# Kernel optimization log

Hardware: AMD Instinct MI355X
Metric: run time of the kernel (lower is better)

## Reference

```python
import jax, jax.numpy as jnp
import numpy as np

NUM_CODES = 8192
EMBED_DIM = 256
N_TOKENS = 65536
COMMITMENT_COST = 0.25


def setup_inputs() -> dict:
    key = jax.random.key(0)
    k1, k2 = jax.random.split(key)
    inputs = jax.random.normal(k1, (N_TOKENS, EMBED_DIM), dtype=jnp.float32)
    # torch init: uniform(-1/num_codes, 1/num_codes); use normal-scale equivalent via uniform
    weight = jax.random.uniform(k2, (NUM_CODES, EMBED_DIM), dtype=jnp.float32,
                                minval=-1.0 / NUM_CODES, maxval=1.0 / NUM_CODES)
    return {"inputs": inputs, "weight": weight}


def reference(inputs, weight):
    inputs_sq = jnp.sum(inputs * inputs, axis=1, keepdims=True)      # (N, 1)
    embed_sq = jnp.sum(weight * weight, axis=1)                      # (K,)
    distances = inputs_sq + embed_sq - 2.0 * (inputs @ weight.T)     # (N, K)
    indices = jnp.argmin(distances, axis=1)                          # (N,)
    quantized = jnp.take(weight, indices, axis=0)                    # (N, D)

    codebook_loss = jnp.mean((quantized - jax.lax.stop_gradient(inputs)) ** 2)
    commit_loss = jnp.mean((inputs - jax.lax.stop_gradient(quantized)) ** 2)
    vq_loss = codebook_loss + COMMITMENT_COST * commit_loss

    # straight-through estimator
    quantized_st = inputs + jax.lax.stop_gradient(quantized - inputs)
    return quantized_st, indices, vq_loss, codebook_loss, commit_loss
```

## Files before the change

### kernel.cpp

```cpp
#include <hip/hip_runtime.h>

#define N_TOK  65536
#define N_CODE 8192
#define DIM    256

typedef _Float16 f16;
typedef _Float16 f16x8 __attribute__((ext_vector_type(8)));
typedef float    f32x4 __attribute__((ext_vector_type(4)));

__global__ __launch_bounds__(256) void rowsq2_kernel(const float* __restrict__ W,
                                                     const float* __restrict__ X,
                                                     float* __restrict__ esq,
                                                     float* __restrict__ sxq) {
    int row  = blockIdx.x * 4 + (threadIdx.x >> 6);
    int lane = threadIdx.x & 63;
    const float* src;
    float* dst;
    if (row < N_CODE) { src = W + (size_t)row * DIM;            dst = esq + row; }
    else              { src = X + (size_t)(row - N_CODE) * DIM; dst = sxq + (row - N_CODE); }
    float4 v = ((const float4*)src)[lane];
    float s = v.x * v.x + v.y * v.y + v.z * v.z + v.w * v.w;
#pragma unroll
    for (int off = 32; off; off >>= 1) s += __shfl_down(s, off, 64);
    if (lane == 0) *dst = s;
}

__global__ __launch_bounds__(256) void splitw_t_kernel(const float* __restrict__ W,
                                                       f16* __restrict__ W1t,
                                                       f16* __restrict__ W2t,
                                                       double* __restrict__ accum) {
    if (blockIdx.x == 0 && threadIdx.x < 128) accum[threadIdx.x] = 0.0;
    int g = blockIdx.x * 256 + threadIdx.x;
    int o = g >> 13;
    int c = g & 8191;
    const float* p = W + (size_t)c * DIM + o * 8;
    float4 v0 = ((const float4*)p)[0];
    float4 v1 = ((const float4*)p)[1];
    float e[8] = {v0.x, v0.y, v0.z, v0.w, v1.x, v1.y, v1.z, v1.w};
    union { f16 h[8]; uint4 u; } p1, p2;
#pragma unroll
    for (int i = 0; i < 8; ++i) {
        float ws = e[i] * 16384.0f;
        f16 w1 = (f16)ws;
        float r = (ws - (float)w1) * 2048.0f;
        p1.h[i] = w1; p2.h[i] = (f16)r;
    }
    size_t byteoff = (size_t)o * 131072 + (size_t)c * 16;
    *(uint4*)((char*)W1t + byteoff) = p1.u;
    *(uint4*)((char*)W2t + byteoff) = p2.u;
}

__global__ __launch_bounds__(256, 2) void argmin_mfma8(
    const float* __restrict__ X, const f16* __restrict__ W1t, const f16* __restrict__ W2t,
    const float* __restrict__ sxq, const float* __restrict__ esq,
    int* __restrict__ out_idx) {

    __shared__ char wbuf[65536];

    const int tid  = threadIdx.x;
    const int lane = tid & 63;
    const int wv   = tid >> 6;
    const int cl   = lane & 15;
    const int q    = lane >> 4;
    const int l5   = lane >> 5;
    const int lane31 = lane & 31;
    const int wavetok0 = blockIdx.x * 128 + wv * 32;

    f16x8 a1[2][8], a2[2][8];
#pragma unroll
    for (int mt = 0; mt < 2; ++mt)
#pragma unroll
        for (int s = 0; s < 8; ++s) {
            const float* p = X + (size_t)(wavetok0 + mt * 16 + cl) * DIM + s * 32 + q * 8;
            float4 v0 = ((const float4*)p)[0];
            float4 v1 = ((const float4*)p)[1];
            float e[8] = {v0.x, v0.y, v0.z, v0.w, v1.x, v1.y, v1.z, v1.w};
#pragma unroll
            for (int j = 0; j < 8; ++j) {
                f16 h = (f16)e[j];
                float r = (e[j] - (float)h) * 2048.0f;
                a1[mt][s][j] = h;
                a2[mt][s][j] = (f16)r;
            }
        }

    float sxr[8];
#pragma unroll
    for (int mt = 0; mt < 2; ++mt)
#pragma unroll
        for (int r = 0; r < 4; ++r)
            sxr[mt * 4 + r] = sxq[wavetok0 + mt * 16 + q * 4 + r];

    float bestd[8];
    int   besti[8];
#pragma unroll
    for (int i = 0; i < 8; ++i) { bestd[i] = 3.4e38f; besti[i] = 0x7fffffff; }

    const int SLB = l5 * 131072 + lane31 * 16;
    const char* RB = wbuf + q * 512 + cl * 16;

    auto stage = [&](int ct2, int sel) {
        const char* g1 = (const char*)W1t + ct2 * 512 + SLB;
        const char* g2 = (const char*)W2t + ct2 * 512 + SLB;
#pragma unroll
        for (int t = 0; t < 8; ++t) {
            int fi = wv * 8 + t;
            int L  = fi >> 4;
            int op = fi & 15;
            const char* gsrc = (L ? g2 : g1) + op * 262144;
            char* ldst = wbuf + sel * 32768 + L * 16384 + op * 1024;
            __builtin_amdgcn_global_load_lds(
                (const __attribute__((address_space(1))) unsigned int*)gsrc,
                (__attribute__((address_space(3))) unsigned int*)ldst, 16, 0, 0);
        }
    };

    stage(0, 0);
    __syncthreads();

    for (int ct = 0; ct < N_CODE / 32; ++ct) {
        if (ct + 1 < N_CODE / 32) stage(ct + 1, (ct + 1) & 1);

        float se0 = esq[ct * 32 + cl];
        float se1 = esq[ct * 32 + 16 + cl];

        f32x4 mainA[2][2], cross[2][2];
#pragma unroll
        for (int mt = 0; mt < 2; ++mt)
#pragma unroll
            for (int nt = 0; nt < 2; ++nt) {
                mainA[mt][nt] = (f32x4){0.f, 0.f, 0.f, 0.f};
                cross[mt][nt] = (f32x4){0.f, 0.f, 0.f, 0.f};
            }

        const char* va = RB + ((ct & 1) << 15);
#pragma unroll
        for (int s = 0; s < 8; ++s) {
            f16x8 b1[2], b2[2];
            b1[0] = *(const f16x8*)(va + s * 2048);
            b1[1] = *(const f16x8*)(va + s * 2048 + 256);
            b2[0] = *(const f16x8*)(va + s * 2048 + 16384);
            b2[1] = *(const f16x8*)(va + s * 2048 + 16640);
            __builtin_amdgcn_s_setprio(1);
#pragma unroll
            for (int mt = 0; mt < 2; ++mt)
#pragma unroll
                for (int nt = 0; nt < 2; ++nt) {
                    mainA[mt][nt] = __builtin_amdgcn_mfma_f32_16x16x32_f16(a1[mt][s], b1[nt], mainA[mt][nt], 0, 0, 0);
                    cross[mt][nt] = __builtin_amdgcn_mfma_f32_16x16x32_f16(a2[mt][s], b1[nt], cross[mt][nt], 0, 0, 0);
                    cross[mt][nt] = __builtin_amdgcn_mfma_f32_16x16x32_f16(a1[mt][s], b2[nt], cross[mt][nt], 0, 0, 0);
                }
            __builtin_amdgcn_s_setprio(0);
        }

#pragma unroll
        for (int mt = 0; mt < 2; ++mt)
#pragma unroll
            for (int nt = 0; nt < 2; ++nt)
#pragma unroll
                for (int r = 0; r < 4; ++r) {
                    float mc = fmaf(cross[mt][nt][r], 4.8828125e-4f, mainA[mt][nt][r]);
                    float t1 = sxr[mt * 4 + r] + (nt ? se1 : se0);
                    float d  = fmaf(-1.220703125e-4f, mc, t1);
                    int slot = mt * 4 + r;
                    if (d < bestd[slot]) {
                        bestd[slot] = d;
                        besti[slot] = ct * 32 + nt * 16 + cl;
                    }
                }
        __syncthreads();
    }

#pragma unroll
    for (int slot = 0; slot < 8; ++slot) {
        float d = bestd[slot];
        int   i = besti[slot];
#pragma unroll
        for (int off = 1; off < 16; off <<= 1) {
            float od = __shfl_xor(d, off, 64);
            int   oi = __shfl_xor(i, off, 64);
            if (od < d || (od == d && oi < i)) { d = od; i = oi; }
        }
        if (cl == 0)
            out_idx[wavetok0 + (slot >> 2) * 16 + q * 4 + (slot & 3)] = i;
    }
}

__global__ __launch_bounds__(256) void finalize_kernel(
    const float* __restrict__ X, const float* __restrict__ W,
    const int* __restrict__ idx, float* __restrict__ outQ,
    float* __restrict__ outI, double* __restrict__ accum) {
    __shared__ double wsum[4];
    int wid  = threadIdx.x >> 6;
    int lane = threadIdx.x & 63;
    int token = blockIdx.x * 4 + wid;
    int id = idx[token];
    float4 x = ((const float4*)(X + (size_t)token * DIM))[lane];
    float4 qv = ((const float4*)(W + (size_t)id * DIM))[lane];
    float4 o;
    o.x = x.x + (qv.x - x.x);
    o.y = x.y + (qv.y - x.y);
    o.z = x.z + (qv.z - x.z);
    o.w = x.w + (qv.w - x.w);
    ((float4*)(outQ + (size_t)token * DIM))[lane] = o;
    float dx = x.x - qv.x, dy = x.y - qv.y, dz = x.z - qv.z, dw = x.w - qv.w;
    float s = dx * dx + dy * dy + dz * dz + dw * dw;
#pragma unroll
    for (int off = 32; off; off >>= 1) s += __shfl_down(s, off, 64);
    if (lane == 0) {
        outI[token] = (float)id;
        wsum[wid] = (double)s;
    }
    __syncthreads();
    if (threadIdx.x == 0) {
        double t = wsum[0] + wsum[1] + wsum[2] + wsum[3];
        atomicAdd(&accum[blockIdx.x & 127], t);
    }
}

__global__ void scalars_kernel(const double* __restrict__ accum, float* __restrict__ out) {
    double mse = 0.0;
    for (int i = 0; i < 128; ++i) mse += accum[i];
    mse /= (double)((size_t)N_TOK * DIM);
    float c = (float)mse;
    out[0] = c + 0.25f * c;
    out[1] = c;
    out[2] = c;
}

extern "C" void kernel_launch(void* const* d_in, const int* in_sizes, int n_in,
                              void* d_out, int out_size, void* d_ws, size_t ws_size,
                              hipStream_t stream) {
    const float* X = (const float*)d_in[0];
    const float* W = (const float*)d_in[1];

    float* outQ = (float*)d_out;
    float* outI = outQ + (size_t)N_TOK * DIM;
    float* outS = outI + N_TOK;

    char* ws = (char*)d_ws;
    double* accum = (double*)ws;
    float* esq = (float*)(ws + 4096);
    float* sxq = (float*)(ws + 4096 + 32768);
    int*   idx = (int*)(ws + 4096 + 32768 + 262144);
    f16*   W1t = (f16*)(ws + (1 << 20));
    f16*   W2t = (f16*)(ws + (1 << 20) + 4194304);

    splitw_t_kernel<<<N_CODE * 32 / 256, 256, 0, stream>>>(W, W1t, W2t, accum);
    rowsq2_kernel<<<(N_CODE + N_TOK) / 4, 256, 0, stream>>>(W, X, esq, sxq);
    argmin_mfma8<<<N_TOK / 128, 256, 0, stream>>>(X, W1t, W2t, sxq, esq, idx);
    finalize_kernel<<<N_TOK / 4, 256, 0, stream>>>(X, W, idx, outQ, outI, accum);
    scalars_kernel<<<1, 1, 0, stream>>>(accum, outS);
}
```

Measured before the change: 766.2 us.

## Fuse prep kernels and fold gather/loss finalize into argmin kernel epilogue

Merges the weight split/transpose and row-norm kernels into one launch by block-index ranges. The gather, straight-through output, index write and squared-error accumulation now run in the epilogue of the argmin MFMA kernel, so the separate finalize kernel and the intermediate index buffer go away. This removes two launches and one round trip of indices through global memory. In exchange the argmin kernel does a serial per-wave loop of 32 token gathers at its tail, which adds memory latency there and may raise register pressure in a kernel bounded to 2 blocks per CU.

```diff
diff --git a/kernel.cpp b/kernel.cpp
--- a/kernel.cpp
+++ b/kernel.cpp
@@ -8,52 +8,54 @@
 typedef _Float16 f16x8 __attribute__((ext_vector_type(8)));
 typedef float    f32x4 __attribute__((ext_vector_type(4)));
 
-__global__ __launch_bounds__(256) void rowsq2_kernel(const float* __restrict__ W,
-                                                     const float* __restrict__ X,
-                                                     float* __restrict__ esq,
-                                                     float* __restrict__ sxq) {
-    int row  = blockIdx.x * 4 + (threadIdx.x >> 6);
-    int lane = threadIdx.x & 63;
-    const float* src;
-    float* dst;
-    if (row < N_CODE) { src = W + (size_t)row * DIM;            dst = esq + row; }
-    else              { src = X + (size_t)(row - N_CODE) * DIM; dst = sxq + (row - N_CODE); }
-    float4 v = ((const float4*)src)[lane];
-    float s = v.x * v.x + v.y * v.y + v.z * v.z + v.w * v.w;
-#pragma unroll
-    for (int off = 32; off; off >>= 1) s += __shfl_down(s, off, 64);
-    if (lane == 0) *dst = s;
-}
-
-__global__ __launch_bounds__(256) void splitw_t_kernel(const float* __restrict__ W,
-                                                       f16* __restrict__ W1t,
-                                                       f16* __restrict__ W2t,
-                                                       double* __restrict__ accum) {
-    if (blockIdx.x == 0 && threadIdx.x < 128) accum[threadIdx.x] = 0.0;
-    int g = blockIdx.x * 256 + threadIdx.x;
-    int o = g >> 13;
-    int c = g & 8191;
-    const float* p = W + (size_t)c * DIM + o * 8;
-    float4 v0 = ((const float4*)p)[0];
-    float4 v1 = ((const float4*)p)[1];
-    float e[8] = {v0.x, v0.y, v0.z, v0.w, v1.x, v1.y, v1.z, v1.w};
-    union { f16 h[8]; uint4 u; } p1, p2;
-#pragma unroll
-    for (int i = 0; i < 8; ++i) {
-        float ws = e[i] * 16384.0f;
-        f16 w1 = (f16)ws;
-        float r = (ws - (float)w1) * 2048.0f;
-        p1.h[i] = w1; p2.h[i] = (f16)r;
+__global__ __launch_bounds__(256) void prep_kernel(const float* __restrict__ W,
+                                                   const float* __restrict__ X,
+                                                   f16* __restrict__ W1t,
+                                                   f16* __restrict__ W2t,
+                                                   float* __restrict__ esq,
+                                                   float* __restrict__ sxq,
+                                                   double* __restrict__ accum) {
+    if (blockIdx.x < 1024) {
+        if (blockIdx.x == 0 && threadIdx.x < 128) accum[threadIdx.x] = 0.0;
+        int g = blockIdx.x * 256 + threadIdx.x;
+        int o = g >> 13;
+        int c = g & 8191;
+        const float* p = W + (size_t)c * DIM + o * 8;
+        float4 v0 = ((const float4*)p)[0];
+        float4 v1 = ((const float4*)p)[1];
+        float e[8] = {v0.x, v0.y, v0.z, v0.w, v1.x, v1.y, v1.z, v1.w};
+        union { f16 h[8]; uint4 u; } p1, p2;
+#pragma unroll
+        for (int i = 0; i < 8; ++i) {
+            float ws = e[i] * 16384.0f;
+            f16 w1 = (f16)ws;
+            float r = (ws - (float)w1) * 2048.0f;
+            p1.h[i] = w1; p2.h[i] = (f16)r;
+        }
+        size_t byteoff = (size_t)o * 131072 + (size_t)c * 16;
+        *(uint4*)((char*)W1t + byteoff) = p1.u;
+        *(uint4*)((char*)W2t + byteoff) = p2.u;
+    } else {
+        int row  = (blockIdx.x - 1024) * 4 + (threadIdx.x >> 6);
+        int lane = threadIdx.x & 63;
+        const float* src;
+        float* dst;
+        if (row < N_CODE) { src = W + (size_t)row * DIM;            dst = esq + row; }
+        else              { src = X + (size_t)(row - N_CODE) * DIM; dst = sxq + (row - N_CODE); }
+        float4 v = ((const float4*)src)[lane];
+        float s = v.x * v.x + v.y * v.y + v.z * v.z + v.w * v.w;
+#pragma unroll
+        for (int off = 32; off; off >>= 1) s += __shfl_down(s, off, 64);
+        if (lane == 0) *dst = s;
     }
-    size_t byteoff = (size_t)o * 131072 + (size_t)c * 16;
-    *(uint4*)((char*)W1t + byteoff) = p1.u;
-    *(uint4*)((char*)W2t + byteoff) = p2.u;
-}
-
-__global__ __launch_bounds__(256, 2) void argmin_mfma8(
-    const float* __restrict__ X, const f16* __restrict__ W1t, const f16* __restrict__ W2t,
+}
+
+__global__ __launch_bounds__(256, 2) void argmin_mfma13(
+    const float* __restrict__ X, const float* __restrict__ W,
+    const f16* __restrict__ W1t, const f16* __restrict__ W2t,
     const float* __restrict__ sxq, const float* __restrict__ esq,
-    int* __restrict__ out_idx) {
+    float* __restrict__ outQ, float* __restrict__ outI,
+    double* __restrict__ accum) {
 
     __shared__ char wbuf[65536];
 
@@ -171,6 +173,7 @@
         __syncthreads();
     }
 
+    int ri[8];
 #pragma unroll
     for (int slot = 0; slot < 8; ++slot) {
         float d = bestd[slot];
@@ -181,41 +184,35 @@
             int   oi = __shfl_xor(i, off, 64);
             if (od < d || (od == d && oi < i)) { d = od; i = oi; }
         }
-        if (cl == 0)
-            out_idx[wavetok0 + (slot >> 2) * 16 + q * 4 + (slot & 3)] = i;
+        ri[slot] = i;
     }
-}
-
-__global__ __launch_bounds__(256) void finalize_kernel(
-    const float* __restrict__ X, const float* __restrict__ W,
-    const int* __restrict__ idx, float* __restrict__ outQ,
-    float* __restrict__ outI, double* __restrict__ accum) {
-    __shared__ double wsum[4];
-    int wid  = threadIdx.x >> 6;
-    int lane = threadIdx.x & 63;
-    int token = blockIdx.x * 4 + wid;
-    int id = idx[token];
-    float4 x = ((const float4*)(X + (size_t)token * DIM))[lane];
-    float4 qv = ((const float4*)(W + (size_t)id * DIM))[lane];
-    float4 o;
-    o.x = x.x + (qv.x - x.x);
-    o.y = x.y + (qv.y - x.y);
-    o.z = x.z + (qv.z - x.z);
-    o.w = x.w + (qv.w - x.w);
-    ((float4*)(outQ + (size_t)token * DIM))[lane] = o;
-    float dx = x.x - qv.x, dy = x.y - qv.y, dz = x.z - qv.z, dw = x.w - qv.w;
-    float s = dx * dx + dy * dy + dz * dz + dw * dw;
-#pragma unroll
-    for (int off = 32; off; off >>= 1) s += __shfl_down(s, off, 64);
-    if (lane == 0) {
-        outI[token] = (float)id;
-        wsum[wid] = (double)s;
-    }
-    __syncthreads();
-    if (threadIdx.x == 0) {
-        double t = wsum[0] + wsum[1] + wsum[2] + wsum[3];
-        atomicAdd(&accum[blockIdx.x & 127], t);
-    }
+
+    double accw = 0.0;
+#pragma unroll
+    for (int slot = 0; slot < 8; ++slot)
+#pragma unroll
+        for (int qq = 0; qq < 4; ++qq) {
+            int id = __shfl(ri[slot], qq * 16);
+            int token = wavetok0 + (slot >> 2) * 16 + qq * 4 + (slot & 3);
+            float4 x  = ((const float4*)(X + (size_t)token * DIM))[lane];
+            float4 qv = ((const float4*)(W + (size_t)id * DIM))[lane];
+            float4 o;
+            o.x = x.x + (qv.x - x.x);
+            o.y = x.y + (qv.y - x.y);
+            o.z = x.z + (qv.z - x.z);
+            o.w = x.w + (qv.w - x.w);
+            ((float4*)(outQ + (size_t)token * DIM))[lane] = o;
+            float dx = x.x - qv.x, dy = x.y - qv.y, dz = x.z - qv.z, dw = x.w - qv.w;
+            float s = dx * dx + dy * dy + dz * dz + dw * dw;
+#pragma unroll
+            for (int off = 32; off; off >>= 1) s += __shfl_down(s, off, 64);
+            if (lane == 0) {
+                outI[token] = (float)id;
+                accw += (double)s;
+            }
+        }
+    if (lane == 0)
+        atomicAdd(&accum[(blockIdx.x * 4 + wv) & 127], accw);
 }
 
 __global__ void scalars_kernel(const double* __restrict__ accum, float* __restrict__ out) {
@@ -242,13 +239,10 @@
     double* accum = (double*)ws;
     float* esq = (float*)(ws + 4096);
     float* sxq = (float*)(ws + 4096 + 32768);
-    int*   idx = (int*)(ws + 4096 + 32768 + 262144);
     f16*   W1t = (f16*)(ws + (1 << 20));
     f16*   W2t = (f16*)(ws + (1 << 20) + 4194304);
 
-    splitw_t_kernel<<<N_CODE * 32 / 256, 256, 0, stream>>>(W, W1t, W2t, accum);
-    rowsq2_kernel<<<(N_CODE + N_TOK) / 4, 256, 0, stream>>>(W, X, esq, sxq);
-    argmin_mfma8<<<N_TOK / 128, 256, 0, stream>>>(X, W1t, W2t, sxq, esq, idx);
-    finalize_kernel<<<N_TOK / 4, 256, 0, stream>>>(X, W, idx, outQ, outI, accum);
+    prep_kernel<<<1024 + (N_CODE + N_TOK) / 4, 256, 0, stream>>>(W, X, W1t, W2t, esq, sxq, accum);
+    argmin_mfma13<<<N_TOK / 128, 256, 0, stream>>>(X, W, W1t, W2t, sxq, esq, outQ, outI, accum);
     scalars_kernel<<<1, 1, 0, stream>>>(accum, outS);
 }
```

Result: no change. 757.1 us (-1.2%).
